# Optimization experiments

Hardware: AMD Instinct MI355X
Metric: run time of the kernel (lower is better)

## Reference

```python
import jax, jax.numpy as jnp
import numpy as np

B, N, M, DIM, H, DH = 2, 2048, 2048, 512, 8, 64
INNER = H * DH  # 512


def setup_inputs() -> dict:
    key = jax.random.key(0)
    ks = jax.random.split(key, 9)
    s = 0.02
    return {
        "x": jax.random.normal(ks[0], (B, N, DIM), jnp.float32),
        "x1": jax.random.normal(ks[1], (B, M, DIM), jnp.float32),
        "attn_mat": jax.random.normal(ks[2], (B, H, N, M), jnp.float32),
        "dots_para": jax.random.uniform(ks[3], (1,), jnp.float32),
        "mat_para": jax.random.uniform(ks[4], (1,), jnp.float32),
        "W_qv": jax.random.normal(ks[5], (DIM, 2 * INNER), jnp.float32) * s,
        "W_k": jax.random.normal(ks[6], (DIM, INNER), jnp.float32) * s,
        "W_out": jax.random.normal(ks[7], (INNER, DIM), jnp.float32) * s,
        "b_out": jax.random.normal(ks[8], (DIM,), jnp.float32) * s,
    }


def _split_heads(t):
    # [b, n, h*d] -> [b, h, n, d]
    b, n, _ = t.shape
    return t.reshape(b, n, H, DH).transpose(0, 2, 1, 3)


def reference(x, x1, attn_mat, dots_para, mat_para, W_qv, W_k, W_out, b_out):
    scale = DH ** -0.5
    qv = x @ W_qv                      # [b, n, 2*inner]
    q, v = jnp.split(qv, 2, axis=-1)
    q = _split_heads(q)                # [b, h, n, d]
    v = _split_heads(v)                # [b, h, n, d]
    k = _split_heads(x1 @ W_k)         # [b, h, m, d]
    dots = jnp.einsum("bhnd,bhmd->bhnm", q, k) * scale
    dots = dots * dots_para + attn_mat * mat_para
    attn = jax.nn.softmax(dots, axis=-1)
    out = jnp.einsum("bhnm,bhmd->bhnd", attn, v)
    out = out.transpose(0, 2, 1, 3).reshape(x.shape[0], x.shape[1], INNER)
    return out @ W_out + b_out
```

## Files before the change

kernel.cpp:

```cpp
#include <hip/hip_runtime.h>
#include <hip/hip_bf16.h>

#define NB 2048
#define MB 2048
#define SPLITS 4
#define MSP (MB / SPLITS)

typedef __attribute__((ext_vector_type(8))) short short8;
typedef __attribute__((ext_vector_type(4))) float floatx4;

__device__ __forceinline__ unsigned short f2bf(float f) {
    union { float f; unsigned int u; } v; v.f = f;
    unsigned int r = (v.u + 0x7FFFu + ((v.u >> 16) & 1u)) >> 16;
    return (unsigned short)r;
}

__device__ __forceinline__ int swz(int row, int k) {
    return (row << 6) + ((((k >> 3) ^ (row & 7))) << 3) + (k & 7);
}
__device__ __forceinline__ int vswz(int row, int k) {
    return (row << 6) + ((((k >> 3) ^ (row & 7) ^ ((row >> 3) & 7))) << 3) + (k & 7);
}

__launch_bounds__(256)
__global__ void prep(const float* __restrict__ x, const float* __restrict__ x1,
                     const float* __restrict__ Wqv, const float* __restrict__ Wk,
                     const float* __restrict__ Wout,
                     unsigned short* __restrict__ xb, unsigned short* __restrict__ x1b,
                     unsigned short* __restrict__ Wqvt, unsigned short* __restrict__ Wkt,
                     unsigned short* __restrict__ Woutt) {
    __shared__ float t[64][65];
    const int bid = blockIdx.x, tid = threadIdx.x;
    if (bid < 2048) {
        const float* in = bid < 1024 ? x : x1;
        unsigned short* out = bid < 1024 ? xb : x1b;
        size_t off = ((size_t)(bid & 1023) * 256 + tid) * 8;
        float4 d0 = *(const float4*)(in + off);
        float4 d1 = *(const float4*)(in + off + 4);
        uint4 o;
        o.x = (unsigned int)f2bf(d0.x) | ((unsigned int)f2bf(d0.y) << 16);
        o.y = (unsigned int)f2bf(d0.z) | ((unsigned int)f2bf(d0.w) << 16);
        o.z = (unsigned int)f2bf(d1.x) | ((unsigned int)f2bf(d1.y) << 16);
        o.w = (unsigned int)f2bf(d1.z) | ((unsigned int)f2bf(d1.w) << 16);
        *(uint4*)(out + off) = o;
        return;
    }
    int tb = bid - 2048;
    const float* W; unsigned short* Wt; int N;
    if (tb < 128)      { W = Wqv;  Wt = Wqvt;  N = 1024; }
    else if (tb < 192) { tb -= 128; W = Wk;   Wt = Wkt;   N = 512; }
    else               { tb -= 192; W = Wout; Wt = Woutt; N = 512; }
    const int k0 = (tb & 7) * 64, n0 = (tb >> 3) * 64;
#pragma unroll
    for (int p = 0; p < 4; p++) {
        int idx = p * 256 + tid;
        int kr = idx >> 4, c4 = (idx & 15) << 2;
        float4 d = *(const float4*)(W + (size_t)(k0 + kr) * N + n0 + c4);
        t[kr][c4 + 0] = d.x; t[kr][c4 + 1] = d.y; t[kr][c4 + 2] = d.z; t[kr][c4 + 3] = d.w;
    }
    __syncthreads();
#pragma unroll
    for (int p = 0; p < 4; p++) {
        int idx = p * 256 + tid;
        int nr = idx >> 4, k4 = (idx & 15) << 2;
        uint2 o;
        o.x = (unsigned int)f2bf(t[k4 + 0][nr]) | ((unsigned int)f2bf(t[k4 + 1][nr]) << 16);
        o.y = (unsigned int)f2bf(t[k4 + 2][nr]) | ((unsigned int)f2bf(t[k4 + 3][nr]) << 16);
        *(uint2*)(Wt + (size_t)(n0 + nr) * 512 + k0 + k4) = o;
    }
}

template <int OUT_BF16>
__device__ __forceinline__ void gemm64_body(const unsigned short* __restrict__ A,
                                            const unsigned short* __restrict__ Bt,
                                            const float* __restrict__ bias,
                                            void* __restrict__ Cp, int Nc, int m0, int n0,
                                            short* Al, short* Bl) {
    const int tid = threadIdx.x;
    const int w = tid >> 6, lane = tid & 63;
    const int quad = lane >> 4, c16 = lane & 15;
    const int wr = (w >> 1) * 32, wc = (w & 1) * 32;

    floatx4 acc[2][2];
#pragma unroll
    for (int i = 0; i < 2; i++)
#pragma unroll
        for (int j = 0; j < 2; j++) acc[i][j] = floatx4{0.f, 0.f, 0.f, 0.f};

    for (int kk = 0; kk < 512; kk += 64) {
        __syncthreads();
#pragma unroll
        for (int p = 0; p < 2; p++) {
            int id = p * 256 + tid;
            int row = id >> 3, c8 = (id & 7) << 3;
            *(uint4*)&Al[swz(row, c8)] = *(const uint4*)(A + (size_t)(m0 + row) * 512 + kk + c8);
            *(uint4*)&Bl[swz(row, c8)] = *(const uint4*)(Bt + (size_t)(n0 + row) * 512 + kk + c8);
        }
        __syncthreads();
#pragma unroll
        for (int kc = 0; kc < 2; kc++) {
            short8 af[2], bf[2];
#pragma unroll
            for (int mt = 0; mt < 2; mt++)
                af[mt] = *(const short8*)&Al[swz(wr + mt * 16 + c16, kc * 32 + quad * 8)];
#pragma unroll
            for (int nt = 0; nt < 2; nt++)
                bf[nt] = *(const short8*)&Bl[swz(wc + nt * 16 + c16, kc * 32 + quad * 8)];
#pragma unroll
            for (int mt = 0; mt < 2; mt++)
#pragma unroll
                for (int nt = 0; nt < 2; nt++)
                    acc[mt][nt] = __builtin_amdgcn_mfma_f32_16x16x32_bf16(af[mt], bf[nt], acc[mt][nt], 0, 0, 0);
        }
    }
#pragma unroll
    for (int mt = 0; mt < 2; mt++)
#pragma unroll
        for (int nt = 0; nt < 2; nt++)
#pragma unroll
            for (int r = 0; r < 4; r++) {
                int row = m0 + wr + mt * 16 + quad * 4 + r;
                int col = n0 + wc + nt * 16 + c16;
                float v = acc[mt][nt][r];
                if (OUT_BF16) {
                    ((unsigned short*)Cp)[(size_t)row * Nc + col] = f2bf(v);
                } else {
                    ((float*)Cp)[(size_t)row * Nc + col] = v + bias[col];
                }
            }
}

__launch_bounds__(256)
__global__ void gemm_qvk(const unsigned short* __restrict__ xb, const unsigned short* __restrict__ x1b,
                         const unsigned short* __restrict__ Wqvt, const unsigned short* __restrict__ Wkt,
                         unsigned short* __restrict__ qvbf, unsigned short* __restrict__ kbf) {
    __shared__ short Al[64 * 64];
    __shared__ short Bl[64 * 64];
    int bid = blockIdx.x;
    if (bid < 1024) {
        gemm64_body<1>(xb, Wqvt, nullptr, qvbf, 1024, (bid & 63) * 64, (bid >> 6) * 64, Al, Bl);
    } else {
        bid -= 1024;
        gemm64_body<1>(x1b, Wkt, nullptr, kbf, 512, (bid & 63) * 64, (bid >> 6) * 64, Al, Bl);
    }
}

__launch_bounds__(256)
__global__ void gemm_out(const unsigned short* __restrict__ A, const unsigned short* __restrict__ Bt,
                         const float* __restrict__ bias, float* __restrict__ C) {
    __shared__ short Al[64 * 64];
    __shared__ short Bl[64 * 64];
    gemm64_body<0>(A, Bt, bias, C, 512, blockIdx.x * 64, blockIdx.y * 64, Al, Bl);
}

__launch_bounds__(256)
__global__ void flash_attn(const unsigned short* __restrict__ qv,
                           const unsigned short* __restrict__ kb,
                           const float* __restrict__ attn_mat,
                           const float* __restrict__ dots_para,
                           const float* __restrict__ mat_para,
                           float* __restrict__ Opart,
                           float* __restrict__ lpart) {
    __shared__ short QP[4][32 * 64];
    __shared__ short Ks[2][64 * 64];
    __shared__ short Vs[2][64 * 64];

    const int tid = threadIdx.x, w = tid >> 6, lane = tid & 63;
    const int quad = lane >> 4, c16 = lane & 15;
    const int q0 = blockIdx.x * 128;
    const int bh = blockIdx.y;
    const int sp = blockIdx.z;
    const int b = bh >> 3, h = bh & 7;
    const int ms = sp * MSP;

    const float log2e = 1.4426950408889634f;
    const float mp = mat_para[0] * log2e;
    const float sdp = dots_para[0] * 0.125f * log2e;

    short* QPf = (short*)QP;
#pragma unroll
    for (int p = 0; p < 4; p++) {
        int id = p * 256 + tid;
        int r = id >> 3, c = id & 7;
        *(uint4*)&QPf[swz(r, c * 8)] =
            *(const uint4*)(qv + (size_t)(b * NB + q0 + r) * 1024 + h * 64 + c * 8);
    }
    __syncthreads();
    short8 qf[2][2];
#pragma unroll
    for (int at = 0; at < 2; at++)
#pragma unroll
        for (int kc = 0; kc < 2; kc++)
            qf[at][kc] = *(const short8*)&QPf[swz(w * 32 + at * 16 + c16, kc * 32 + quad * 8)];
    short* Pw = &QPf[w * 2048];

    const int sr = tid >> 3, sc = tid & 7;
    uint4 kreg[2], vreg[2];
    auto loadKV = [&](int m) {
#pragma unroll
        for (int p = 0; p < 2; p++) {
            int r = p * 32 + sr;
            kreg[p] = *(const uint4*)(kb + (size_t)(b * MB + m + r) * 512 + h * 64 + sc * 8);
            vreg[p] = *(const uint4*)(qv + (size_t)(b * NB + m + r) * 1024 + 512 + h * 64 + sc * 8);
        }
    };
    auto storeKV = [&](int bufi) {
#pragma unroll
        for (int p = 0; p < 2; p++) {
            int r = p * 32 + sr;
            *(uint4*)&Ks[bufi][swz(r, sc * 8)] = kreg[p];
            uint4 d = vreg[p];
            Vs[bufi][vswz(sc * 8 + 0, r)] = (short)(d.x & 0xffff);
            Vs[bufi][vswz(sc * 8 + 1, r)] = (short)(d.x >> 16);
            Vs[bufi][vswz(sc * 8 + 2, r)] = (short)(d.y & 0xffff);
            Vs[bufi][vswz(sc * 8 + 3, r)] = (short)(d.y >> 16);
            Vs[bufi][vswz(sc * 8 + 4, r)] = (short)(d.z & 0xffff);
            Vs[bufi][vswz(sc * 8 + 5, r)] = (short)(d.z >> 16);
            Vs[bufi][vswz(sc * 8 + 6, r)] = (short)(d.w & 0xffff);
            Vs[bufi][vswz(sc * 8 + 7, r)] = (short)(d.w >> 16);
        }
    };
    const float* amp = attn_mat + ((size_t)bh * NB + q0 + w * 32 + quad * 4) * MB + c16;
    float amr[2][4][4];
    auto loadAM = [&](int m0_) {
#pragma unroll
        for (int at = 0; at < 2; at++)
#pragma unroll
            for (int r = 0; r < 4; r++)
#pragma unroll
                for (int t = 0; t < 4; t++)
                    amr[at][t][r] = amp[(size_t)(at * 16 + r) * MB + m0_ + t * 16];
    };

    loadKV(ms);
    storeKV(0);
    loadKV(ms + 64 < ms + MSP ? ms + 64 : ms);
    loadAM(ms);

    floatx4 O[2][4];
    float l[2][4];
#pragma unroll
    for (int at = 0; at < 2; at++)
#pragma unroll
        for (int i = 0; i < 4; i++) { O[at][i] = floatx4{0.f, 0.f, 0.f, 0.f}; l[at][i] = 0.f; }

    for (int it = 0; it < MSP / 64; it++) {
        const int m0 = ms + it * 64;
        const int buf = it & 1, nbuf = buf ^ 1;
        __syncthreads();
        storeKV(nbuf);
        int mnn = m0 + 128; if (mnn >= ms + MSP) mnn = ms;
        loadKV(mnn);

        floatx4 S[2][4];
#pragma unroll
        for (int t = 0; t < 4; t++) {
            short8 kf0 = *(const short8*)&Ks[buf][swz(t * 16 + c16, quad * 8)];
            short8 kf1 = *(const short8*)&Ks[buf][swz(t * 16 + c16, 32 + quad * 8)];
#pragma unroll
            for (int at = 0; at < 2; at++) {
                floatx4 s = floatx4{0.f, 0.f, 0.f, 0.f};
                s = __builtin_amdgcn_mfma_f32_16x16x32_bf16(qf[at][0], kf0, s, 0, 0, 0);
                s = __builtin_amdgcn_mfma_f32_16x16x32_bf16(qf[at][1], kf1, s, 0, 0, 0);
                S[at][t] = s;
            }
        }

#pragma unroll
        for (int at = 0; at < 2; at++)
#pragma unroll
            for (int t = 0; t < 4; t++)
#pragma unroll
                for (int r = 0; r < 4; r++) {
                    float p = exp2f(fmaf(S[at][t][r], sdp, amr[at][t][r] * mp));
                    l[at][r] += p;
                    Pw[swz(at * 16 + quad * 4 + r, t * 16 + c16)] = (short)f2bf(p);
                }
        int mnx = m0 + 64; if (mnx >= ms + MSP) mnx = ms;
        loadAM(mnx);
        __threadfence_block();

        short8 pf[2][2];
#pragma unroll
        for (int at = 0; at < 2; at++)
#pragma unroll
            for (int kc = 0; kc < 2; kc++)
                pf[at][kc] = *(const short8*)&Pw[swz(at * 16 + c16, kc * 32 + quad * 8)];
#pragma unroll
        for (int dt = 0; dt < 4; dt++) {
            short8 vf0 = *(const short8*)&Vs[buf][vswz(dt * 16 + c16, quad * 8)];
            short8 vf1 = *(const short8*)&Vs[buf][vswz(dt * 16 + c16, 32 + quad * 8)];
#pragma unroll
            for (int at = 0; at < 2; at++) {
                O[at][dt] = __builtin_amdgcn_mfma_f32_16x16x32_bf16(pf[at][0], vf0, O[at][dt], 0, 0, 0);
                O[at][dt] = __builtin_amdgcn_mfma_f32_16x16x32_bf16(pf[at][1], vf1, O[at][dt], 0, 0, 0);
            }
        }
    }

#pragma unroll
    for (int at = 0; at < 2; at++) {
#pragma unroll
        for (int r = 0; r < 4; r++) {
            float s = l[at][r];
            s += __shfl_xor(s, 1);
            s += __shfl_xor(s, 2);
            s += __shfl_xor(s, 4);
            s += __shfl_xor(s, 8);
            l[at][r] = s;
        }
        if (c16 == 0) {
#pragma unroll
            for (int r = 0; r < 4; r++)
                lpart[(size_t)(sp * 16 + bh) * NB + q0 + w * 32 + at * 16 + quad * 4 + r] = l[at][r];
        }
#pragma unroll
        for (int dt = 0; dt < 4; dt++)
#pragma unroll
            for (int r = 0; r < 4; r++) {
                size_t row = (size_t)sp * 4096 + b * NB + q0 + w * 32 + at * 16 + quad * 4 + r;
                Opart[row * 512 + h * 64 + dt * 16 + c16] = O[at][dt][r];
            }
    }
}

__launch_bounds__(256)
__global__ void combine_splits(const float* __restrict__ Opart, const float* __restrict__ lpart,
                               unsigned short* __restrict__ ao) {
    int idx = blockIdx.x * 256 + threadIdx.x;
    int row = idx >> 7;
    int col = (idx & 127) << 2;
    int b = row >> 11, n = row & 2047, h = col >> 6;
    float ls = 0.f;
    float4 o = {0.f, 0.f, 0.f, 0.f};
#pragma unroll
    for (int sp = 0; sp < SPLITS; sp++) {
        ls += lpart[(size_t)(sp * 16 + b * 8 + h) * NB + n];
        float4 os = *(const float4*)(Opart + ((size_t)sp * 4096 + row) * 512 + col);
        o.x += os.x; o.y += os.y; o.z += os.z; o.w += os.w;
    }
    float rinv = 1.0f / ls;
    uint2 pk;
    pk.x = (unsigned int)f2bf(o.x * rinv) | ((unsigned int)f2bf(o.y * rinv) << 16);
    pk.y = (unsigned int)f2bf(o.z * rinv) | ((unsigned int)f2bf(o.w * rinv) << 16);
    *(uint2*)(ao + (size_t)row * 512 + col) = pk;
}

extern "C" void kernel_launch(void* const* d_in, const int* in_sizes, int n_in,
                              void* d_out, int out_size, void* d_ws, size_t ws_size,
                              hipStream_t stream) {
    const float* x         = (const float*)d_in[0];
    const float* x1        = (const float*)d_in[1];
    const float* attn_mat  = (const float*)d_in[2];
    const float* dots_para = (const float*)d_in[3];
    const float* mat_para  = (const float*)d_in[4];
    const float* W_qv      = (const float*)d_in[5];
    const float* W_k       = (const float*)d_in[6];
    const float* W_out     = (const float*)d_in[7];
    const float* b_out     = (const float*)d_in[8];
    float* out = (float*)d_out;

    unsigned short* xb    = (unsigned short*)d_ws;
    unsigned short* x1b   = xb    + (size_t)4096 * 512;
    unsigned short* qvbf  = x1b   + (size_t)4096 * 512;
    unsigned short* kbf   = qvbf  + (size_t)4096 * 1024;
    unsigned short* aobf  = kbf   + (size_t)4096 * 512;
    unsigned short* Wqvt  = aobf  + (size_t)4096 * 512;
    unsigned short* Wkt   = Wqvt  + (size_t)1024 * 512;
    unsigned short* Woutt = Wkt   + (size_t)512 * 512;
    float*          Opart = (float*)(Woutt + (size_t)512 * 512);
    float*          lpart = Opart + (size_t)SPLITS * 4096 * 512;

    dim3 blk(256);
    prep<<<2304, blk, 0, stream>>>(x, x1, W_qv, W_k, W_out, xb, x1b, Wqvt, Wkt, Woutt);
    gemm_qvk<<<1536, blk, 0, stream>>>(xb, x1b, Wqvt, Wkt, qvbf, kbf);
    flash_attn<<<dim3(16, 16, SPLITS), blk, 0, stream>>>(qvbf, kbf, attn_mat, dots_para, mat_para, Opart, lpart);
    combine_splits<<<2048, blk, 0, stream>>>(Opart, lpart, aobf);
    gemm_out<<<dim3(64, 8), blk, 0, stream>>>(aobf, Woutt, b_out, out);
}
```

Before: 449.8 us.

## Fuse split-K combine into attention via last-block atomic counter, use three splits

The combine_splits kernel is removed. Each attention block writes its partial O and row sums into a per-thread-contiguous scratch layout, then bumps a per-tile atomic counter. The last arriving split sums the other splits, normalizes, and writes the bf16 output directly. The split count also drops from 4 to 3 uneven chunks (11/11/10 tiles), giving 768 blocks to reduce partial traffic and launch overhead, at the cost of grid/CU balance and a serialized tail reduction.

```diff
diff --git a/kernel.cpp b/kernel.cpp
--- a/kernel.cpp
+++ b/kernel.cpp
@@ -3,8 +3,7 @@
 
 #define NB 2048
 #define MB 2048
-#define SPLITS 4
-#define MSP (MB / SPLITS)
+#define SPLITS 3
 
 typedef __attribute__((ext_vector_type(8))) short short8;
 typedef __attribute__((ext_vector_type(4))) float floatx4;
@@ -28,9 +27,10 @@
                      const float* __restrict__ Wout,
                      unsigned short* __restrict__ xb, unsigned short* __restrict__ x1b,
                      unsigned short* __restrict__ Wqvt, unsigned short* __restrict__ Wkt,
-                     unsigned short* __restrict__ Woutt) {
+                     unsigned short* __restrict__ Woutt, unsigned int* __restrict__ cnt) {
     __shared__ float t[64][65];
     const int bid = blockIdx.x, tid = threadIdx.x;
+    if (bid == 0 && tid < 256) cnt[tid] = 0;
     if (bid < 2048) {
         const float* in = bid < 1024 ? x : x1;
         unsigned short* out = bid < 1024 ? xb : x1b;
@@ -159,11 +159,14 @@
                            const float* __restrict__ attn_mat,
                            const float* __restrict__ dots_para,
                            const float* __restrict__ mat_para,
-                           float* __restrict__ Opart,
-                           float* __restrict__ lpart) {
+                           float* __restrict__ Obuf,
+                           float* __restrict__ lpart,
+                           unsigned int* __restrict__ cnt,
+                           unsigned short* __restrict__ aobf) {
     __shared__ short QP[4][32 * 64];
     __shared__ short Ks[2][64 * 64];
     __shared__ short Vs[2][64 * 64];
+    __shared__ unsigned int is_last;
 
     const int tid = threadIdx.x, w = tid >> 6, lane = tid & 63;
     const int quad = lane >> 4, c16 = lane & 15;
@@ -171,7 +174,9 @@
     const int bh = blockIdx.y;
     const int sp = blockIdx.z;
     const int b = bh >> 3, h = bh & 7;
-    const int ms = sp * MSP;
+    const int t0 = sp * 11;
+    const int ntl = (sp == 2) ? 10 : 11;
+    const int ms = t0 * 64;
 
     const float log2e = 1.4426950408889634f;
     const float mp = mat_para[0] * log2e;
@@ -234,7 +239,7 @@
 
     loadKV(ms);
     storeKV(0);
-    loadKV(ms + 64 < ms + MSP ? ms + 64 : ms);
+    loadKV(ms + 64);
     loadAM(ms);
 
     floatx4 O[2][4];
@@ -244,13 +249,13 @@
 #pragma unroll
         for (int i = 0; i < 4; i++) { O[at][i] = floatx4{0.f, 0.f, 0.f, 0.f}; l[at][i] = 0.f; }
 
-    for (int it = 0; it < MSP / 64; it++) {
-        const int m0 = ms + it * 64;
+    for (int it = 0; it < ntl; it++) {
+        const int m0 = (t0 + it) * 64;
         const int buf = it & 1, nbuf = buf ^ 1;
         __syncthreads();
         storeKV(nbuf);
-        int mnn = m0 + 128; if (mnn >= ms + MSP) mnn = ms;
-        loadKV(mnn);
+        int i2 = it + 2;
+        loadKV((i2 < ntl ? t0 + i2 : t0) * 64);
 
         floatx4 S[2][4];
 #pragma unroll
@@ -276,8 +281,8 @@
                     l[at][r] += p;
                     Pw[swz(at * 16 + quad * 4 + r, t * 16 + c16)] = (short)f2bf(p);
                 }
-        int mnx = m0 + 64; if (mnx >= ms + MSP) mnx = ms;
-        loadAM(mnx);
+        int i1 = it + 1;
+        loadAM((i1 < ntl ? t0 + i1 : t0) * 64);
         __threadfence_block();
 
         short8 pf[2][2];
@@ -299,7 +304,7 @@
     }
 
 #pragma unroll
-    for (int at = 0; at < 2; at++) {
+    for (int at = 0; at < 2; at++)
 #pragma unroll
         for (int r = 0; r < 4; r++) {
             float s = l[at][r];
@@ -309,41 +314,63 @@
             s += __shfl_xor(s, 8);
             l[at][r] = s;
         }
-        if (c16 == 0) {
+
+    const int tk = blockIdx.x * 16 + bh;
+    float* ob = Obuf + ((size_t)sp * 256 + tk) * (256 * 32) + tid * 32;
+#pragma unroll
+    for (int at = 0; at < 2; at++)
+#pragma unroll
+        for (int dt = 0; dt < 4; dt++)
+            *(float4*)(ob + at * 16 + dt * 4) = *(float4*)&O[at][dt];
+    if (c16 == 0) {
+#pragma unroll
+        for (int at = 0; at < 2; at++)
 #pragma unroll
             for (int r = 0; r < 4; r++)
-                lpart[(size_t)(sp * 16 + bh) * NB + q0 + w * 32 + at * 16 + quad * 4 + r] = l[at][r];
-        }
+                lpart[((size_t)sp * 256 + tk) * 128 + w * 32 + at * 16 + quad * 4 + r] = l[at][r];
+    }
+
+    __threadfence();
+    __syncthreads();
+    if (tid == 0) {
+        unsigned int old = atomicAdd(&cnt[tk], 1u);
+        is_last = (old == SPLITS - 1) ? 1u : 0u;
+    }
+    __syncthreads();
+    if (!is_last) return;
+    __threadfence();
+
+#pragma unroll
+    for (int s2 = 1; s2 < SPLITS; s2++) {
+        int sp2 = sp + s2; if (sp2 >= SPLITS) sp2 -= SPLITS;
+        const float* ob2 = Obuf + ((size_t)sp2 * 256 + tk) * (256 * 32) + tid * 32;
+#pragma unroll
+        for (int at = 0; at < 2; at++)
+#pragma unroll
+            for (int dt = 0; dt < 4; dt++) {
+                float4 o2 = *(const float4*)(ob2 + at * 16 + dt * 4);
+                O[at][dt][0] += o2.x; O[at][dt][1] += o2.y;
+                O[at][dt][2] += o2.z; O[at][dt][3] += o2.w;
+            }
+#pragma unroll
+        for (int at = 0; at < 2; at++)
+#pragma unroll
+            for (int r = 0; r < 4; r++)
+                l[at][r] += lpart[((size_t)sp2 * 256 + tk) * 128 + w * 32 + at * 16 + quad * 4 + r];
+    }
+#pragma unroll
+    for (int at = 0; at < 2; at++) {
+        float rinv[4];
+#pragma unroll
+        for (int r = 0; r < 4; r++) rinv[r] = 1.0f / l[at][r];
 #pragma unroll
         for (int dt = 0; dt < 4; dt++)
 #pragma unroll
             for (int r = 0; r < 4; r++) {
-                size_t row = (size_t)sp * 4096 + b * NB + q0 + w * 32 + at * 16 + quad * 4 + r;
-                Opart[row * 512 + h * 64 + dt * 16 + c16] = O[at][dt][r];
+                size_t row = (size_t)b * NB + q0 + w * 32 + at * 16 + quad * 4 + r;
+                aobf[row * 512 + h * 64 + dt * 16 + c16] = f2bf(O[at][dt][r] * rinv[r]);
             }
     }
-}
-
-__launch_bounds__(256)
-__global__ void combine_splits(const float* __restrict__ Opart, const float* __restrict__ lpart,
-                               unsigned short* __restrict__ ao) {
-    int idx = blockIdx.x * 256 + threadIdx.x;
-    int row = idx >> 7;
-    int col = (idx & 127) << 2;
-    int b = row >> 11, n = row & 2047, h = col >> 6;
-    float ls = 0.f;
-    float4 o = {0.f, 0.f, 0.f, 0.f};
-#pragma unroll
-    for (int sp = 0; sp < SPLITS; sp++) {
-        ls += lpart[(size_t)(sp * 16 + b * 8 + h) * NB + n];
-        float4 os = *(const float4*)(Opart + ((size_t)sp * 4096 + row) * 512 + col);
-        o.x += os.x; o.y += os.y; o.z += os.z; o.w += os.w;
-    }
-    float rinv = 1.0f / ls;
-    uint2 pk;
-    pk.x = (unsigned int)f2bf(o.x * rinv) | ((unsigned int)f2bf(o.y * rinv) << 16);
-    pk.y = (unsigned int)f2bf(o.z * rinv) | ((unsigned int)f2bf(o.w * rinv) << 16);
-    *(uint2*)(ao + (size_t)row * 512 + col) = pk;
 }
 
 extern "C" void kernel_launch(void* const* d_in, const int* in_sizes, int n_in,
@@ -368,13 +395,14 @@
     unsigned short* Wqvt  = aobf  + (size_t)4096 * 512;
     unsigned short* Wkt   = Wqvt  + (size_t)1024 * 512;
     unsigned short* Woutt = Wkt   + (size_t)512 * 512;
-    float*          Opart = (float*)(Woutt + (size_t)512 * 512);
-    float*          lpart = Opart + (size_t)SPLITS * 4096 * 512;
+    float*          Obuf  = (float*)(Woutt + (size_t)512 * 512);
+    float*          lpart = Obuf + (size_t)SPLITS * 256 * 256 * 32;
+    unsigned int*   cnt   = (unsigned int*)(lpart + (size_t)SPLITS * 256 * 128);
 
     dim3 blk(256);
-    prep<<<2304, blk, 0, stream>>>(x, x1, W_qv, W_k, W_out, xb, x1b, Wqvt, Wkt, Woutt);
+    prep<<<2304, blk, 0, stream>>>(x, x1, W_qv, W_k, W_out, xb, x1b, Wqvt, Wkt, Woutt, cnt);
     gemm_qvk<<<1536, blk, 0, stream>>>(xb, x1b, Wqvt, Wkt, qvbf, kbf);
-    flash_attn<<<dim3(16, 16, SPLITS), blk, 0, stream>>>(qvbf, kbf, attn_mat, dots_para, mat_para, Opart, lpart);
-    combine_splits<<<2048, blk, 0, stream>>>(Opart, lpart, aobf);
+    flash_attn<<<dim3(16, 16, SPLITS), blk, 0, stream>>>(qvbf, kbf, attn_mat, dots_para, mat_para,
+                                                         Obuf, lpart, cnt, aobf);
     gemm_out<<<dim3(64, 8), blk, 0, stream>>>(aobf, Woutt, b_out, out);
 }
```

Result: slower. 662.9 us (+47.4%).

## Write V transposed per head from the projection GEMM to avoid LDS scatter

Applied to the files above, without the earlier changes.

The QV projection GEMM now writes the V half directly in a transposed [b,h,d,n] bf16 layout. The flash attention kernel loads V with contiguous 16-byte vectors and stores it to LDS as a single vector write with the standard swizzle. This replaces the previous per-element scattered 2-byte LDS transpose stores. The cost is strided 8-byte global writes in the GEMM epilogue and a separate workspace buffer. The prefetch wraparound guard on the second KV load is also dropped.

```diff
diff --git a/kernel.cpp b/kernel.cpp
--- a/kernel.cpp
+++ b/kernel.cpp
@@ -17,9 +17,6 @@
 
 __device__ __forceinline__ int swz(int row, int k) {
     return (row << 6) + ((((k >> 3) ^ (row & 7))) << 3) + (k & 7);
-}
-__device__ __forceinline__ int vswz(int row, int k) {
-    return (row << 6) + ((((k >> 3) ^ (row & 7) ^ ((row >> 3) & 7))) << 3) + (k & 7);
 }
 
 __launch_bounds__(256)
@@ -70,7 +67,7 @@
     }
 }
 
-template <int OUT_BF16>
+template <int MODE>
 __device__ __forceinline__ void gemm64_body(const unsigned short* __restrict__ A,
                                             const unsigned short* __restrict__ Bt,
                                             const float* __restrict__ bias,
@@ -116,29 +113,46 @@
 #pragma unroll
     for (int mt = 0; mt < 2; mt++)
 #pragma unroll
-        for (int nt = 0; nt < 2; nt++)
-#pragma unroll
-            for (int r = 0; r < 4; r++) {
-                int row = m0 + wr + mt * 16 + quad * 4 + r;
-                int col = n0 + wc + nt * 16 + c16;
-                float v = acc[mt][nt][r];
-                if (OUT_BF16) {
-                    ((unsigned short*)Cp)[(size_t)row * Nc + col] = f2bf(v);
-                } else {
-                    ((float*)Cp)[(size_t)row * Nc + col] = v + bias[col];
+        for (int nt = 0; nt < 2; nt++) {
+            if (MODE == 2) {
+                int col2 = n0 + wc + nt * 16 + c16 - 512;
+                int hh = col2 >> 6, dd = col2 & 63;
+                int row0 = m0 + wr + mt * 16 + quad * 4;
+                int bb = row0 >> 11, nb = row0 & 2047;
+                uint2 o;
+                o.x = (unsigned int)f2bf(acc[mt][nt][0]) | ((unsigned int)f2bf(acc[mt][nt][1]) << 16);
+                o.y = (unsigned int)f2bf(acc[mt][nt][2]) | ((unsigned int)f2bf(acc[mt][nt][3]) << 16);
+                *(uint2*)((unsigned short*)Cp + ((size_t)((bb * 8 + hh) * 64 + dd)) * 2048 + nb) = o;
+            } else {
+#pragma unroll
+                for (int r = 0; r < 4; r++) {
+                    int row = m0 + wr + mt * 16 + quad * 4 + r;
+                    int col = n0 + wc + nt * 16 + c16;
+                    float v = acc[mt][nt][r];
+                    if (MODE == 1) {
+                        ((unsigned short*)Cp)[(size_t)row * Nc + col] = f2bf(v);
+                    } else {
+                        ((float*)Cp)[(size_t)row * Nc + col] = v + bias[col];
+                    }
                 }
             }
+        }
 }
 
 __launch_bounds__(256)
 __global__ void gemm_qvk(const unsigned short* __restrict__ xb, const unsigned short* __restrict__ x1b,
                          const unsigned short* __restrict__ Wqvt, const unsigned short* __restrict__ Wkt,
-                         unsigned short* __restrict__ qvbf, unsigned short* __restrict__ kbf) {
+                         unsigned short* __restrict__ qvbf, unsigned short* __restrict__ vt,
+                         unsigned short* __restrict__ kbf) {
     __shared__ short Al[64 * 64];
     __shared__ short Bl[64 * 64];
     int bid = blockIdx.x;
     if (bid < 1024) {
-        gemm64_body<1>(xb, Wqvt, nullptr, qvbf, 1024, (bid & 63) * 64, (bid >> 6) * 64, Al, Bl);
+        int m0 = (bid & 63) * 64, n0 = (bid >> 6) * 64;
+        if (n0 < 512)
+            gemm64_body<1>(xb, Wqvt, nullptr, qvbf, 1024, m0, n0, Al, Bl);
+        else
+            gemm64_body<2>(xb, Wqvt, nullptr, vt, 1024, m0, n0, Al, Bl);
     } else {
         bid -= 1024;
         gemm64_body<1>(x1b, Wkt, nullptr, kbf, 512, (bid & 63) * 64, (bid >> 6) * 64, Al, Bl);
@@ -156,6 +170,7 @@
 __launch_bounds__(256)
 __global__ void flash_attn(const unsigned short* __restrict__ qv,
                            const unsigned short* __restrict__ kb,
+                           const unsigned short* __restrict__ vt,
                            const float* __restrict__ attn_mat,
                            const float* __restrict__ dots_para,
                            const float* __restrict__ mat_para,
@@ -195,13 +210,14 @@
     short* Pw = &QPf[w * 2048];
 
     const int sr = tid >> 3, sc = tid & 7;
+    const unsigned short* vbase = vt + (size_t)((b * 8 + h) * 64) * 2048;
     uint4 kreg[2], vreg[2];
     auto loadKV = [&](int m) {
 #pragma unroll
         for (int p = 0; p < 2; p++) {
             int r = p * 32 + sr;
             kreg[p] = *(const uint4*)(kb + (size_t)(b * MB + m + r) * 512 + h * 64 + sc * 8);
-            vreg[p] = *(const uint4*)(qv + (size_t)(b * NB + m + r) * 1024 + 512 + h * 64 + sc * 8);
+            vreg[p] = *(const uint4*)(vbase + (size_t)r * 2048 + m + sc * 8);
         }
     };
     auto storeKV = [&](int bufi) {
@@ -209,15 +225,7 @@
         for (int p = 0; p < 2; p++) {
             int r = p * 32 + sr;
             *(uint4*)&Ks[bufi][swz(r, sc * 8)] = kreg[p];
-            uint4 d = vreg[p];
-            Vs[bufi][vswz(sc * 8 + 0, r)] = (short)(d.x & 0xffff);
-            Vs[bufi][vswz(sc * 8 + 1, r)] = (short)(d.x >> 16);
-            Vs[bufi][vswz(sc * 8 + 2, r)] = (short)(d.y & 0xffff);
-            Vs[bufi][vswz(sc * 8 + 3, r)] = (short)(d.y >> 16);
-            Vs[bufi][vswz(sc * 8 + 4, r)] = (short)(d.z & 0xffff);
-            Vs[bufi][vswz(sc * 8 + 5, r)] = (short)(d.z >> 16);
-            Vs[bufi][vswz(sc * 8 + 6, r)] = (short)(d.w & 0xffff);
-            Vs[bufi][vswz(sc * 8 + 7, r)] = (short)(d.w >> 16);
+            *(uint4*)&Vs[bufi][swz(r, sc * 8)] = vreg[p];
         }
     };
     const float* amp = attn_mat + ((size_t)bh * NB + q0 + w * 32 + quad * 4) * MB + c16;
@@ -234,7 +242,7 @@
 
     loadKV(ms);
     storeKV(0);
-    loadKV(ms + 64 < ms + MSP ? ms + 64 : ms);
+    loadKV(ms + 64);
     loadAM(ms);
 
     floatx4 O[2][4];
@@ -288,8 +296,8 @@
                 pf[at][kc] = *(const short8*)&Pw[swz(at * 16 + c16, kc * 32 + quad * 8)];
 #pragma unroll
         for (int dt = 0; dt < 4; dt++) {
-            short8 vf0 = *(const short8*)&Vs[buf][vswz(dt * 16 + c16, quad * 8)];
-            short8 vf1 = *(const short8*)&Vs[buf][vswz(dt * 16 + c16, 32 + quad * 8)];
+            short8 vf0 = *(const short8*)&Vs[buf][swz(dt * 16 + c16, quad * 8)];
+            short8 vf1 = *(const short8*)&Vs[buf][swz(dt * 16 + c16, 32 + quad * 8)];
 #pragma unroll
             for (int at = 0; at < 2; at++) {
                 O[at][dt] = __builtin_amdgcn_mfma_f32_16x16x32_bf16(pf[at][0], vf0, O[at][dt], 0, 0, 0);
@@ -363,7 +371,8 @@
     unsigned short* xb    = (unsigned short*)d_ws;
     unsigned short* x1b   = xb    + (size_t)4096 * 512;
     unsigned short* qvbf  = x1b   + (size_t)4096 * 512;
-    unsigned short* kbf   = qvbf  + (size_t)4096 * 1024;
+    unsigned short* vt    = qvbf  + (size_t)4096 * 1024;
+    unsigned short* kbf   = vt    + (size_t)2 * 8 * 64 * 2048;
     unsigned short* aobf  = kbf   + (size_t)4096 * 512;
     unsigned short* Wqvt  = aobf  + (size_t)4096 * 512;
     unsigned short* Wkt   = Wqvt  + (size_t)1024 * 512;
@@ -373,8 +382,9 @@
 
     dim3 blk(256);
     prep<<<2304, blk, 0, stream>>>(x, x1, W_qv, W_k, W_out, xb, x1b, Wqvt, Wkt, Woutt);
-    gemm_qvk<<<1536, blk, 0, stream>>>(xb, x1b, Wqvt, Wkt, qvbf, kbf);
-    flash_attn<<<dim3(16, 16, SPLITS), blk, 0, stream>>>(qvbf, kbf, attn_mat, dots_para, mat_para, Opart, lpart);
+    gemm_qvk<<<1536, blk, 0, stream>>>(xb, x1b, Wqvt, Wkt, qvbf, vt, kbf);
+    flash_attn<<<dim3(16, 16, SPLITS), blk, 0, stream>>>(qvbf, kbf, vt, attn_mat, dots_para, mat_para,
+                                                         Opart, lpart);
     combine_splits<<<2048, blk, 0, stream>>>(Opart, lpart, aobf);
     gemm_out<<<dim3(64, 8), blk, 0, stream>>>(aobf, Woutt, b_out, out);
 }
```

New measurement: 464.0 us. 3.1% more time.
